# Kernel optimization log

Measured on AMD Instinct MI355X. Metric: run time of the kernel, lower is better.

The kernel has to match this reference:

```python
import jax, jax.numpy as jnp
import numpy as np

K = 2  # top-k experts kept


def setup_inputs() -> dict:
    key = jax.random.key(0)
    k1, k2, k3 = jax.random.split(key, 3)
    M, B, D, H = 8, 8192, 1024, 256
    zs = jax.random.normal(k1, (M, B, D), dtype=jnp.float32)
    W1 = jax.random.normal(k2, (M * D, H), dtype=jnp.float32) * 0.02
    b1 = jnp.zeros((H,), dtype=jnp.float32)
    W2 = jax.random.normal(k3, (H, M), dtype=jnp.float32) * 0.02
    b2 = jnp.zeros((M,), dtype=jnp.float32)
    return {"zs": zs, "W1": W1, "b1": b1, "W2": W2, "b2": b2}


def reference(zs, W1, b1, W2, b2):
    M, B, D = zs.shape
    # torch.cat(zs, dim=-1) -> [B, M*D]
    cat = jnp.transpose(zs, (1, 0, 2)).reshape(B, M * D)
    # gate MLP: Linear -> GELU(exact) -> Linear
    h = jax.nn.gelu(cat @ W1 + b1, approximate=False)
    logits = h @ W2 + b2                      # [B, M]
    # eval path: no noise added
    topk_logits, topk_idx = jax.lax.top_k(logits, K)  # [B, K]
    topk_w = jax.nn.softmax(topk_logits, axis=-1)     # [B, K]
    # scatter top-k weights into dense [B, M] routing matrix
    rows = jnp.arange(B)[:, None]
    w = jnp.zeros_like(logits).at[rows, topk_idx].set(topk_w)
    # fused = sum_i zs[i] * w[:, i:i+1]
    fused = jnp.einsum("mbd,bm->bd", zs, w)
    return fused, w
```

## Files before the change

kernel.cpp:

```cpp
#include <hip/hip_runtime.h>
#include <math.h>

constexpr int B_ = 8192;
constexpr int D_ = 1024;
constexpr int M_ = 8;
constexpr int H_ = 256;

constexpr int SPLITK = 4;
constexpr int KSP = 2048;
constexpr int BM = 64, BK = 16;
constexpr int NCH = KSP / BK;
constexpr int NG  = (M_ * D_) / BK;

typedef __bf16 bf16x8 __attribute__((ext_vector_type(8)));
typedef float  f32x16 __attribute__((ext_vector_type(16)));
typedef short  short8 __attribute__((ext_vector_type(8)));
typedef short  short4v __attribute__((ext_vector_type(4)));

__device__ __forceinline__ unsigned short f2bf(float x) {
    unsigned int u = __float_as_uint(x);
    u += 0x7FFFu + ((u >> 16) & 1u);
    return (unsigned short)(u >> 16);
}
__device__ __forceinline__ float bf2f(unsigned short s) {
    return __uint_as_float(((unsigned int)s) << 16);
}

#define MFMA(A, Bf, C) __builtin_amdgcn_mfma_f32_32x32x16_bf16((A), (Bf), (C), 0, 0, 0)

#define GLOAD_LDS16(gp, lp)                                                    \
    __builtin_amdgcn_global_load_lds(                                          \
        (const __attribute__((address_space(1))) void*)(gp),                   \
        (__attribute__((address_space(3))) void*)(lp), 16, 0, 0)

__global__ __launch_bounds__(256)
void splitw1_kernel(const float* __restrict__ W1, short* __restrict__ Ph,
                    short* __restrict__ Pm, short* __restrict__ Pl)
{
    const int g = blockIdx.x;
    const int t = threadIdx.x;
    float v[16];
#pragma unroll
    for (int k = 0; k < 16; ++k) v[k] = W1[(size_t)(g * 16 + k) * H_ + t];
#pragma unroll
    for (int ks = 0; ks < 2; ++ks) {
        short8 vh, vm, vl;
#pragma unroll
        for (int j = 0; j < 8; ++j) {
            const float x = v[ks * 8 + j];
            const unsigned short h = f2bf(x);
            float r = x - bf2f(h);
            const unsigned short m = f2bf(r);
            r = r - bf2f(m);
            const unsigned short l = f2bf(r);
            vh[j] = (short)h; vm[j] = (short)m; vl[j] = (short)l;
        }
        const size_t o = ((size_t)(g * 2 + ks) * 256 + t) * 8;
        *(short8*)&Ph[o] = vh;
        *(short8*)&Pm[o] = vm;
        *(short8*)&Pl[o] = vl;
    }
}

__global__ __launch_bounds__(256, 2)
void gemm1_kernel(const float* __restrict__ zs,
                  const short* __restrict__ Ph,
                  const short* __restrict__ Pm,
                  const short* __restrict__ Pl,
                  float* __restrict__ part)
{
    __shared__ short Ah[2][1024], Am_[2][1024], Al[2][1024];
    __shared__ short Bh[2][4096], Bm_[2][4096], Bl[2][4096];

    const int t  = threadIdx.x;
    const int b0 = blockIdx.x * BM;
    const int g0 = blockIdx.y * NCH;

    const int ar  = t >> 2;
    const int ap  = t & 3;
    const int aof = ((ap >> 1) * 64 + ar) * 8 + (ap & 1) * 4;

    const int lane = t & 63;
    const int wv   = t >> 6;
    const int kl   = lane >> 5;
    const int ln   = lane & 31;

    f32x16 acc[4];
#pragma unroll
    for (int i = 0; i < 4; ++i) acc[i] = (f32x16)0.0f;

    float4 areg;

#define STAGE_B(BUF, G) {                                                      \
    _Pragma("unroll")                                                          \
    for (int ks = 0; ks < 2; ++ks) {                                           \
        const size_t so = (((size_t)(G) * 2 + ks) * 256 + t) * 8;              \
        const int   dof = (ks * 256 + t) * 8;                                  \
        GLOAD_LDS16(Ph + so, &Bh[BUF][dof]);                                   \
        GLOAD_LDS16(Pm + so, &Bm_[BUF][dof]);                                  \
        GLOAD_LDS16(Pl + so, &Bl[BUF][dof]);                                   \
    }                                                                          \
}

#define LOAD_A(G) {                                                            \
    const int kg = (G) * 16;                                                   \
    areg = *(const float4*)(zs + ((size_t)(kg >> 10) * B_ + b0 + ar) * D_      \
                               + (kg & 1023) + ap * 4);                        \
}

#define STORE_A(BUF) {                                                         \
    const float av[4] = {areg.x, areg.y, areg.z, areg.w};                      \
    short4v vh, vm, vl;                                                        \
    _Pragma("unroll")                                                          \
    for (int j = 0; j < 4; ++j) {                                              \
        const unsigned short h = f2bf(av[j]);                                  \
        float r = av[j] - bf2f(h);                                             \
        const unsigned short m = f2bf(r);                                      \
        r = r - bf2f(m);                                                       \
        const unsigned short l = f2bf(r);                                      \
        vh[j] = (short)h; vm[j] = (short)m; vl[j] = (short)l;                  \
    }                                                                          \
    *(short4v*)&Ah[BUF][aof]  = vh;                                            \
    *(short4v*)&Am_[BUF][aof] = vm;                                            \
    *(short4v*)&Al[BUF][aof]  = vl;                                            \
}

    STAGE_B(0, g0)
    LOAD_A(g0)
    STORE_A(0)
    __syncthreads();

    int buf = 0;
#pragma unroll 1
    for (int c = 0; c < NCH; ++c) {
        if (c + 1 < NCH) {
            STAGE_B(buf ^ 1, g0 + c + 1)
            LOAD_A(g0 + c + 1)
        }
        {
            const int ib = (kl * 256 + wv * 64 + ln) * 8;
            const bf16x8 bh0 = __builtin_bit_cast(bf16x8, *(const short8*)&Bh[buf][ib]);
            const bf16x8 bm0 = __builtin_bit_cast(bf16x8, *(const short8*)&Bm_[buf][ib]);
            const bf16x8 bl0 = __builtin_bit_cast(bf16x8, *(const short8*)&Bl[buf][ib]);
            const bf16x8 bh1 = __builtin_bit_cast(bf16x8, *(const short8*)&Bh[buf][ib + 256]);
            const bf16x8 bm1 = __builtin_bit_cast(bf16x8, *(const short8*)&Bm_[buf][ib + 256]);
            const bf16x8 bl1 = __builtin_bit_cast(bf16x8, *(const short8*)&Bl[buf][ib + 256]);
            const int ia = (kl * 64 + ln) * 8;
            const bf16x8 ah0 = __builtin_bit_cast(bf16x8, *(const short8*)&Ah[buf][ia]);
            const bf16x8 am0 = __builtin_bit_cast(bf16x8, *(const short8*)&Am_[buf][ia]);
            const bf16x8 al0 = __builtin_bit_cast(bf16x8, *(const short8*)&Al[buf][ia]);
            const bf16x8 ah1 = __builtin_bit_cast(bf16x8, *(const short8*)&Ah[buf][ia + 256]);
            const bf16x8 am1 = __builtin_bit_cast(bf16x8, *(const short8*)&Am_[buf][ia + 256]);
            const bf16x8 al1 = __builtin_bit_cast(bf16x8, *(const short8*)&Al[buf][ia + 256]);
            acc[0] = MFMA(ah0, bh0, acc[0]); acc[1] = MFMA(ah0, bh1, acc[1]);
            acc[2] = MFMA(ah1, bh0, acc[2]); acc[3] = MFMA(ah1, bh1, acc[3]);
            acc[0] = MFMA(ah0, bm0, acc[0]); acc[1] = MFMA(ah0, bm1, acc[1]);
            acc[2] = MFMA(ah1, bm0, acc[2]); acc[3] = MFMA(ah1, bm1, acc[3]);
            acc[0] = MFMA(am0, bh0, acc[0]); acc[1] = MFMA(am0, bh1, acc[1]);
            acc[2] = MFMA(am1, bh0, acc[2]); acc[3] = MFMA(am1, bh1, acc[3]);
            acc[0] = MFMA(am0, bm0, acc[0]); acc[1] = MFMA(am0, bm1, acc[1]);
            acc[2] = MFMA(am1, bm0, acc[2]); acc[3] = MFMA(am1, bm1, acc[3]);
            acc[0] = MFMA(ah0, bl0, acc[0]); acc[1] = MFMA(ah0, bl1, acc[1]);
            acc[2] = MFMA(ah1, bl0, acc[2]); acc[3] = MFMA(ah1, bl1, acc[3]);
            acc[0] = MFMA(al0, bh0, acc[0]); acc[1] = MFMA(al0, bh1, acc[1]);
            acc[2] = MFMA(al1, bh0, acc[2]); acc[3] = MFMA(al1, bh1, acc[3]);
        }
        if (c + 1 < NCH) STORE_A(buf ^ 1)
        __syncthreads();
        buf ^= 1;
    }
#undef STAGE_B
#undef LOAD_A
#undef STORE_A

    float* P = part + ((size_t)blockIdx.y * B_ + b0) * H_;
#pragma unroll
    for (int rt = 0; rt < 2; ++rt) {
#pragma unroll
        for (int ctl = 0; ctl < 2; ++ctl) {
            const f32x16 v = acc[rt * 2 + ctl];
            const int col = wv * 64 + ctl * 32 + ln;
#pragma unroll
            for (int r = 0; r < 16; ++r) {
                const int row = rt * 32 + (r & 3) + 8 * (r >> 2) + 4 * kl;
                P[(size_t)row * H_ + col] = v[r];
            }
        }
    }
}

__device__ __forceinline__ float gelu_exact(float x) {
    return 0.5f * x * (1.0f + erff(x * 0.70710678118654752f));
}

__global__ __launch_bounds__(256)
void gate_combine_kernel(const float* __restrict__ part, const float* __restrict__ b1,
                         const float* __restrict__ W2, const float* __restrict__ b2,
                         const float* __restrict__ zs, float* __restrict__ fused,
                         float* __restrict__ w_out)
{
    const int t    = threadIdx.x;
    const int wv   = t >> 6;
    const int lane = t & 63;
    const int row  = blockIdx.x * 4 + wv;

    const float* pr = part + (size_t)row * H_ + lane * 4;
    const float4 x0 = *(const float4*)pr;
    const float4 x1 = *(const float4*)(pr + (size_t)B_ * H_);
    const float4 x2 = *(const float4*)(pr + (size_t)2 * B_ * H_);
    const float4 x3 = *(const float4*)(pr + (size_t)3 * B_ * H_);
    const float4 bb = *(const float4*)&b1[lane * 4];
    const float h0 = gelu_exact(x0.x + x1.x + x2.x + x3.x + bb.x);
    const float h1 = gelu_exact(x0.y + x1.y + x2.y + x3.y + bb.y);
    const float h2 = gelu_exact(x0.z + x1.z + x2.z + x3.z + bb.z);
    const float h3 = gelu_exact(x0.w + x1.w + x2.w + x3.w + bb.w);

    float lg[8] = {0, 0, 0, 0, 0, 0, 0, 0};
    const int cb = lane * 4;
#define ACC8(HC, CI) {                                                         \
    const float4 wa_ = *(const float4*)&W2[(cb + (CI)) * 8];                   \
    const float4 wb_ = *(const float4*)&W2[(cb + (CI)) * 8 + 4];               \
    lg[0] = fmaf((HC), wa_.x, lg[0]); lg[1] = fmaf((HC), wa_.y, lg[1]);        \
    lg[2] = fmaf((HC), wa_.z, lg[2]); lg[3] = fmaf((HC), wa_.w, lg[3]);        \
    lg[4] = fmaf((HC), wb_.x, lg[4]); lg[5] = fmaf((HC), wb_.y, lg[5]);        \
    lg[6] = fmaf((HC), wb_.z, lg[6]); lg[7] = fmaf((HC), wb_.w, lg[7]);        \
}
    ACC8(h0, 0) ACC8(h1, 1) ACC8(h2, 2) ACC8(h3, 3)
#undef ACC8

#pragma unroll
    for (int off = 32; off >= 1; off >>= 1) {
#pragma unroll
        for (int i = 0; i < 8; ++i) lg[i] += __shfl_xor(lg[i], off, 64);
    }

    float l[8];
#pragma unroll
    for (int i = 0; i < 8; ++i) l[i] = lg[i] + b2[i];
    int i1 = 0; float l1 = l[0];
#pragma unroll
    for (int i = 1; i < 8; ++i) if (l[i] > l1) { l1 = l[i]; i1 = i; }
    int i2 = (i1 == 0) ? 1 : 0; float l2 = l[i2];
#pragma unroll
    for (int i = 0; i < 8; ++i)
        if (i != i1 && l[i] > l2) { l2 = l[i]; i2 = i; }

    const float e  = expf(l2 - l1);
    const float dn = 1.0f + e;
    const float wa = 1.0f / dn;
    const float wb = e / dn;

    if (lane == 0) {
        float* wr = w_out + (size_t)row * M_;
#pragma unroll
        for (int i = 0; i < 8; ++i)
            wr[i] = (i == i1) ? wa : ((i == i2) ? wb : 0.0f);
    }

    const float4* z1 = (const float4*)(zs + ((size_t)i1 * B_ + row) * D_);
    const float4* z2 = (const float4*)(zs + ((size_t)i2 * B_ + row) * D_);
    float4* o = (float4*)(fused + (size_t)row * D_);
#pragma unroll
    for (int i = 0; i < 4; ++i) {
        const int d = lane + i * 64;
        const float4 x = z1[d];
        const float4 y = z2[d];
        o[d] = make_float4(fmaf(wa, x.x, wb * y.x),
                           fmaf(wa, x.y, wb * y.y),
                           fmaf(wa, x.z, wb * y.z),
                           fmaf(wa, x.w, wb * y.w));
    }
}

extern "C" void kernel_launch(void* const* d_in, const int* in_sizes, int n_in,
                              void* d_out, int out_size, void* d_ws, size_t ws_size,
                              hipStream_t stream)
{
    const float* zs = (const float*)d_in[0];
    const float* W1 = (const float*)d_in[1];
    const float* b1 = (const float*)d_in[2];
    const float* W2 = (const float*)d_in[3];
    const float* b2 = (const float*)d_in[4];

    float* fused = (float*)d_out;
    float* w_out = fused + (size_t)B_ * D_;

    float* part = (float*)d_ws;
    short* Ph = (short*)(part + (size_t)SPLITK * B_ * H_);
    const size_t PSZ = (size_t)NG * 2 * 256 * 8;
    short* Pm = Ph + PSZ;
    short* Pl = Pm + PSZ;

    splitw1_kernel<<<NG, 256, 0, stream>>>(W1, Ph, Pm, Pl);
    gemm1_kernel<<<dim3(B_ / BM, SPLITK), 256, 0, stream>>>(zs, Ph, Pm, Pl, part);
    gate_combine_kernel<<<dim3(B_ / 4), 256, 0, stream>>>(part, b1, W2, b2, zs, fused, w_out);
}
```

Before: 528.7 us.

## Load W1 split fragments directly into registers with 512-thread blocks

The GEMM1 kernel no longer stages the bf16 hi/mid/lo W1 pieces through LDS. Each of 8 waves now loads its own 32-column B fragment straight from global memory into registers, with register double-buffering and a loop unrolled by two. Block size doubles to 512 threads so every wave owns one 32-column slice, and each thread loads and splits two zs floats instead of four. This removes LDS traffic and LDS capacity for B, which should allow more resident blocks. In exchange, global loads are no longer async LDS copies, and per-wave MFMA work per sync shrinks.

```diff
diff --git a/kernel.cpp b/kernel.cpp
--- a/kernel.cpp
+++ b/kernel.cpp
@@ -15,7 +15,7 @@
 typedef __bf16 bf16x8 __attribute__((ext_vector_type(8)));
 typedef float  f32x16 __attribute__((ext_vector_type(16)));
 typedef short  short8 __attribute__((ext_vector_type(8)));
-typedef short  short4v __attribute__((ext_vector_type(4)));
+typedef short  short2v __attribute__((ext_vector_type(2)));
 
 __device__ __forceinline__ unsigned short f2bf(float x) {
     unsigned int u = __float_as_uint(x);
@@ -27,11 +27,6 @@
 }
 
 #define MFMA(A, Bf, C) __builtin_amdgcn_mfma_f32_32x32x16_bf16((A), (Bf), (C), 0, 0, 0)
-
-#define GLOAD_LDS16(gp, lp)                                                    \
-    __builtin_amdgcn_global_load_lds(                                          \
-        (const __attribute__((address_space(1))) void*)(gp),                   \
-        (__attribute__((address_space(3))) void*)(lp), 16, 0, 0)
 
 __global__ __launch_bounds__(256)
 void splitw1_kernel(const float* __restrict__ W1, short* __restrict__ Ph,
@@ -62,7 +57,7 @@
     }
 }
 
-__global__ __launch_bounds__(256, 2)
+__global__ __launch_bounds__(512, 4)
 void gemm1_kernel(const float* __restrict__ zs,
                   const short* __restrict__ Ph,
                   const short* __restrict__ Pm,
@@ -70,122 +65,116 @@
                   float* __restrict__ part)
 {
     __shared__ short Ah[2][1024], Am_[2][1024], Al[2][1024];
-    __shared__ short Bh[2][4096], Bm_[2][4096], Bl[2][4096];
 
     const int t  = threadIdx.x;
-    const int b0 = blockIdx.x * BM;
+    const int bb0 = blockIdx.x * BM;
     const int g0 = blockIdx.y * NCH;
 
-    const int ar  = t >> 2;
-    const int ap  = t & 3;
-    const int aof = ((ap >> 1) * 64 + ar) * 8 + (ap & 1) * 4;
+    const int ar  = t >> 3;
+    const int ap  = t & 7;
+    const int aof = ((ap >> 2) * 64 + ar) * 8 + (ap & 3) * 2;
 
     const int lane = t & 63;
     const int wv   = t >> 6;
     const int kl   = lane >> 5;
     const int ln   = lane & 31;
 
-    f32x16 acc[4];
-#pragma unroll
-    for (int i = 0; i < 4; ++i) acc[i] = (f32x16)0.0f;
-
-    float4 areg;
-
-#define STAGE_B(BUF, G) {                                                      \
-    _Pragma("unroll")                                                          \
-    for (int ks = 0; ks < 2; ++ks) {                                           \
-        const size_t so = (((size_t)(G) * 2 + ks) * 256 + t) * 8;              \
-        const int   dof = (ks * 256 + t) * 8;                                  \
-        GLOAD_LDS16(Ph + so, &Bh[BUF][dof]);                                   \
-        GLOAD_LDS16(Pm + so, &Bm_[BUF][dof]);                                  \
-        GLOAD_LDS16(Pl + so, &Bl[BUF][dof]);                                   \
-    }                                                                          \
-}
+    f32x16 acc0 = (f32x16)0.0f;
+    f32x16 acc1 = (f32x16)0.0f;
+
+    unsigned ob = ((unsigned)(g0 * 2 + kl) * 256u + (unsigned)(wv * 32 + ln)) * 8u;
+    const int ia = (kl * 64 + ln) * 8;
+
+    float2 areg;
 
 #define LOAD_A(G) {                                                            \
     const int kg = (G) * 16;                                                   \
-    areg = *(const float4*)(zs + ((size_t)(kg >> 10) * B_ + b0 + ar) * D_      \
-                               + (kg & 1023) + ap * 4);                        \
+    areg = *(const float2*)(zs + ((size_t)(kg >> 10) * B_ + bb0 + ar) * D_     \
+                               + (kg & 1023) + ap * 2);                        \
 }
 
 #define STORE_A(BUF) {                                                         \
-    const float av[4] = {areg.x, areg.y, areg.z, areg.w};                      \
-    short4v vh, vm, vl;                                                        \
-    _Pragma("unroll")                                                          \
-    for (int j = 0; j < 4; ++j) {                                              \
-        const unsigned short h = f2bf(av[j]);                                  \
-        float r = av[j] - bf2f(h);                                             \
-        const unsigned short m = f2bf(r);                                      \
-        r = r - bf2f(m);                                                       \
+    short2v vh, vm, vl;                                                        \
+    {                                                                          \
+        const float x = areg.x;                                                \
+        const unsigned short h = f2bf(x); float r = x - bf2f(h);               \
+        const unsigned short m = f2bf(r); r = r - bf2f(m);                     \
         const unsigned short l = f2bf(r);                                      \
-        vh[j] = (short)h; vm[j] = (short)m; vl[j] = (short)l;                  \
+        vh[0] = (short)h; vm[0] = (short)m; vl[0] = (short)l;                  \
     }                                                                          \
-    *(short4v*)&Ah[BUF][aof]  = vh;                                            \
-    *(short4v*)&Am_[BUF][aof] = vm;                                            \
-    *(short4v*)&Al[BUF][aof]  = vl;                                            \
-}
-
-    STAGE_B(0, g0)
+    {                                                                          \
+        const float x = areg.y;                                                \
+        const unsigned short h = f2bf(x); float r = x - bf2f(h);               \
+        const unsigned short m = f2bf(r); r = r - bf2f(m);                     \
+        const unsigned short l = f2bf(r);                                      \
+        vh[1] = (short)h; vm[1] = (short)m; vl[1] = (short)l;                  \
+    }                                                                          \
+    *(short2v*)&Ah[BUF][aof]  = vh;                                            \
+    *(short2v*)&Am_[BUF][aof] = vm;                                            \
+    *(short2v*)&Al[BUF][aof]  = vl;                                            \
+}
+
+#define LOAD_B(DH, DM, DL, OFF) {                                              \
+    DH = *(const short8*)&Ph[OFF];                                             \
+    DM = *(const short8*)&Pm[OFF];                                             \
+    DL = *(const short8*)&Pl[OFF];                                             \
+}
+
+#define COMPUTE(BUF, RH, RM, RL) {                                             \
+    const bf16x8 vbh = __builtin_bit_cast(bf16x8, RH);                         \
+    const bf16x8 vbm = __builtin_bit_cast(bf16x8, RM);                         \
+    const bf16x8 vbl = __builtin_bit_cast(bf16x8, RL);                         \
+    const bf16x8 ah0 = __builtin_bit_cast(bf16x8, *(const short8*)&Ah[BUF][ia]);        \
+    const bf16x8 am0 = __builtin_bit_cast(bf16x8, *(const short8*)&Am_[BUF][ia]);       \
+    const bf16x8 al0 = __builtin_bit_cast(bf16x8, *(const short8*)&Al[BUF][ia]);        \
+    const bf16x8 ah1 = __builtin_bit_cast(bf16x8, *(const short8*)&Ah[BUF][ia + 256]);  \
+    const bf16x8 am1 = __builtin_bit_cast(bf16x8, *(const short8*)&Am_[BUF][ia + 256]); \
+    const bf16x8 al1 = __builtin_bit_cast(bf16x8, *(const short8*)&Al[BUF][ia + 256]);  \
+    acc0 = MFMA(ah0, vbh, acc0); acc1 = MFMA(ah1, vbh, acc1);                  \
+    acc0 = MFMA(ah0, vbm, acc0); acc1 = MFMA(ah1, vbm, acc1);                  \
+    acc0 = MFMA(am0, vbh, acc0); acc1 = MFMA(am1, vbh, acc1);                  \
+    acc0 = MFMA(am0, vbm, acc0); acc1 = MFMA(am1, vbm, acc1);                  \
+    acc0 = MFMA(ah0, vbl, acc0); acc1 = MFMA(ah1, vbl, acc1);                  \
+    acc0 = MFMA(al0, vbh, acc0); acc1 = MFMA(al1, vbh, acc1);                  \
+}
+
+    short8 sAh, sAm, sAl, sBh, sBm, sBl;
+
+    LOAD_B(sAh, sAm, sAl, ob)
     LOAD_A(g0)
     STORE_A(0)
     __syncthreads();
 
-    int buf = 0;
 #pragma unroll 1
-    for (int c = 0; c < NCH; ++c) {
-        if (c + 1 < NCH) {
-            STAGE_B(buf ^ 1, g0 + c + 1)
-            LOAD_A(g0 + c + 1)
+    for (int c = 0; c < NCH; c += 2) {
+        ob += 4096;
+        LOAD_B(sBh, sBm, sBl, ob)
+        LOAD_A(g0 + c + 1)
+        COMPUTE(0, sAh, sAm, sAl)
+        STORE_A(1)
+        __syncthreads();
+
+        if (c + 2 < NCH) {
+            ob += 4096;
+            LOAD_B(sAh, sAm, sAl, ob)
+            LOAD_A(g0 + c + 2)
         }
-        {
-            const int ib = (kl * 256 + wv * 64 + ln) * 8;
-            const bf16x8 bh0 = __builtin_bit_cast(bf16x8, *(const short8*)&Bh[buf][ib]);
-            const bf16x8 bm0 = __builtin_bit_cast(bf16x8, *(const short8*)&Bm_[buf][ib]);
-            const bf16x8 bl0 = __builtin_bit_cast(bf16x8, *(const short8*)&Bl[buf][ib]);
-            const bf16x8 bh1 = __builtin_bit_cast(bf16x8, *(const short8*)&Bh[buf][ib + 256]);
-            const bf16x8 bm1 = __builtin_bit_cast(bf16x8, *(const short8*)&Bm_[buf][ib + 256]);
-            const bf16x8 bl1 = __builtin_bit_cast(bf16x8, *(const short8*)&Bl[buf][ib + 256]);
-            const int ia = (kl * 64 + ln) * 8;
-            const bf16x8 ah0 = __builtin_bit_cast(bf16x8, *(const short8*)&Ah[buf][ia]);
-            const bf16x8 am0 = __builtin_bit_cast(bf16x8, *(const short8*)&Am_[buf][ia]);
-            const bf16x8 al0 = __builtin_bit_cast(bf16x8, *(const short8*)&Al[buf][ia]);
-            const bf16x8 ah1 = __builtin_bit_cast(bf16x8, *(const short8*)&Ah[buf][ia + 256]);
-            const bf16x8 am1 = __builtin_bit_cast(bf16x8, *(const short8*)&Am_[buf][ia + 256]);
-            const bf16x8 al1 = __builtin_bit_cast(bf16x8, *(const short8*)&Al[buf][ia + 256]);
-            acc[0] = MFMA(ah0, bh0, acc[0]); acc[1] = MFMA(ah0, bh1, acc[1]);
-            acc[2] = MFMA(ah1, bh0, acc[2]); acc[3] = MFMA(ah1, bh1, acc[3]);
-            acc[0] = MFMA(ah0, bm0, acc[0]); acc[1] = MFMA(ah0, bm1, acc[1]);
-            acc[2] = MFMA(ah1, bm0, acc[2]); acc[3] = MFMA(ah1, bm1, acc[3]);
-            acc[0] = MFMA(am0, bh0, acc[0]); acc[1] = MFMA(am0, bh1, acc[1]);
-            acc[2] = MFMA(am1, bh0, acc[2]); acc[3] = MFMA(am1, bh1, acc[3]);
-            acc[0] = MFMA(am0, bm0, acc[0]); acc[1] = MFMA(am0, bm1, acc[1]);
-            acc[2] = MFMA(am1, bm0, acc[2]); acc[3] = MFMA(am1, bm1, acc[3]);
-            acc[0] = MFMA(ah0, bl0, acc[0]); acc[1] = MFMA(ah0, bl1, acc[1]);
-            acc[2] = MFMA(ah1, bl0, acc[2]); acc[3] = MFMA(ah1, bl1, acc[3]);
-            acc[0] = MFMA(al0, bh0, acc[0]); acc[1] = MFMA(al0, bh1, acc[1]);
-            acc[2] = MFMA(al1, bh0, acc[2]); acc[3] = MFMA(al1, bh1, acc[3]);
-        }
-        if (c + 1 < NCH) STORE_A(buf ^ 1)
+        COMPUTE(1, sBh, sBm, sBl)
+        if (c + 2 < NCH) STORE_A(0)
         __syncthreads();
-        buf ^= 1;
-    }
-#undef STAGE_B
+    }
 #undef LOAD_A
 #undef STORE_A
-
-    float* P = part + ((size_t)blockIdx.y * B_ + b0) * H_;
-#pragma unroll
-    for (int rt = 0; rt < 2; ++rt) {
-#pragma unroll
-        for (int ctl = 0; ctl < 2; ++ctl) {
-            const f32x16 v = acc[rt * 2 + ctl];
-            const int col = wv * 64 + ctl * 32 + ln;
-#pragma unroll
-            for (int r = 0; r < 16; ++r) {
-                const int row = rt * 32 + (r & 3) + 8 * (r >> 2) + 4 * kl;
-                P[(size_t)row * H_ + col] = v[r];
-            }
-        }
+#undef LOAD_B
+#undef COMPUTE
+
+    float* P = part + ((size_t)blockIdx.y * B_ + bb0) * H_;
+    const int col = wv * 32 + ln;
+#pragma unroll
+    for (int r = 0; r < 16; ++r) {
+        const int row0 = (r & 3) + 8 * (r >> 2) + 4 * kl;
+        P[(size_t)row0 * H_ + col]        = acc0[r];
+        P[(size_t)(row0 + 32) * H_ + col] = acc1[r];
     }
 }
 
@@ -292,6 +281,6 @@
     short* Pl = Pm + PSZ;
 
     splitw1_kernel<<<NG, 256, 0, stream>>>(W1, Ph, Pm, Pl);
-    gemm1_kernel<<<dim3(B_ / BM, SPLITK), 256, 0, stream>>>(zs, Ph, Pm, Pl, part);
+    gemm1_kernel<<<dim3(B_ / BM, SPLITK), 512, 0, stream>>>(zs, Ph, Pm, Pl, part);
     gate_combine_kernel<<<dim3(B_ / 4), 256, 0, stream>>>(part, b1, W2, b2, zs, fused, w_out);
 }
```

Result: faster. 505.7 us (-4.4%).
